# Kernel optimization log

Hardware: AMD Instinct MI355X
Metric: run time of the kernel (lower is better)

The kernel has to match this reference:

```python
import jax, jax.numpy as jnp
import numpy as np

N_RAYS, N_SAMPLES, WIDTH = 4096, 192, 128


def _linear_params(key, fan_in, fan_out):
    # torch nn.Linear default init: U(-1/sqrt(fan_in), 1/sqrt(fan_in))
    kw, kb = jax.random.split(key)
    s = 1.0 / np.sqrt(fan_in)
    w = jax.random.uniform(kw, (fan_in, fan_out), minval=-s, maxval=s, dtype=jnp.float32)
    b = jax.random.uniform(kb, (fan_out,), minval=-s, maxval=s, dtype=jnp.float32)
    return w, b


def setup_inputs() -> dict:
    key = jax.random.key(0)
    ks = jax.random.split(key, 9)
    w0, b0 = _linear_params(ks[0], 3, WIDTH)            # feature layer 0
    w1, b1 = _linear_params(ks[1], WIDTH, WIDTH)        # feature layer 1
    w2, b2 = _linear_params(ks[2], WIDTH + 3, WIDTH)    # feature layer 2 (skip concat)
    w3, b3 = _linear_params(ks[3], WIDTH, WIDTH)        # feature layer 3
    wd, bd = _linear_params(ks[4], WIDTH, 1)            # density head
    wf, bf = _linear_params(ks[5], WIDTH, WIDTH)        # feature head
    wr, br = _linear_params(ks[6], WIDTH + 3, WIDTH // 2)  # rgb layer
    wo, bo = _linear_params(ks[7], WIDTH // 2, 3)       # rgb head
    x = jax.random.normal(ks[8], (N_RAYS, N_SAMPLES, 6), dtype=jnp.float32)
    return dict(x=x, w0=w0, b0=b0, w1=w1, b1=b1, w2=w2, b2=b2, w3=w3, b3=b3,
                wd=wd, bd=bd, wf=wf, bf=bf, wr=wr, br=br, wo=wo, bo=bo)


def reference(x, w0, b0, w1, b1, w2, b2, w3, b3, wd, bd, wf, bf, wr, br, wo, bo):
    relu = jax.nn.relu
    position, view_dir = x[..., :3], x[..., 3:]
    h = relu(position @ w0 + b0)                                   # [R,S,128]
    h = relu(h @ w1 + b1)
    h = relu(jnp.concatenate([h, position], axis=-1) @ w2 + b2)    # skip at i=2
    h = relu(h @ w3 + b3)
    density = relu(h @ wd + bd)                                    # [R,S,1]
    features = relu(h @ wf + bf)                                   # [R,S,128]
    r = relu(jnp.concatenate([features, view_dir], axis=-1) @ wr + br)  # [R,S,64]
    rgb = jax.nn.sigmoid(r @ wo + bo)                              # [R,S,3]
    return (rgb, density)
```

## Files before the change

### kernel.cpp

```cpp
#include <hip/hip_runtime.h>
#include <hip/hip_bf16.h>

#define N_PTS (4096 * 192)
#define NT 4

typedef __bf16 bf16x8 __attribute__((ext_vector_type(8)));
typedef float  f32x4  __attribute__((ext_vector_type(4)));
typedef float  f32x2  __attribute__((ext_vector_type(2)));

#define W1P 0
#define W2P 16384
#define W3P 32768
#define WFP 49152
#define WRP 65536
#define W0E 73728
#define W2E 75776
#define WRE 77824
#define WDE 78848
#define WOE 79104

__device__ __forceinline__ int kinv(int k) {
  int c = k >> 5, q = (k >> 3) & 3, h = (k >> 2) & 1, r = k & 3;
  return (2 * c + h) * 16 + q * 4 + r;
}

__global__ void prep_kernel(const float* __restrict__ w0, const float* __restrict__ w1,
                            const float* __restrict__ w2, const float* __restrict__ w3,
                            const float* __restrict__ wf, const float* __restrict__ wr,
                            const float* __restrict__ wd, const float* __restrict__ wo,
                            __bf16* __restrict__ ws) {
  int i = blockIdx.x * 256 + threadIdx.x;
  if (i < 65536) {
    int t = i >> 14, j = i & 16383, m = j >> 7, col = j & 127;
    int k = (((col >> 3) ^ (m & 15)) << 3) | (col & 7);
    int p = kinv(k);
    const float* w = (t == 0) ? w1 : (t == 1) ? w2 : (t == 2) ? w3 : wf;
    ws[i] = (__bf16)w[p * 128 + m];
  } else if (i < 73728) {
    int j = i - 65536, m = j >> 7, col = j & 127;
    int k = (((col >> 3) ^ (m & 15)) << 3) | (col & 7);
    int p = kinv(k);
    ws[i] = (__bf16)wr[p * 64 + m];
  } else if (i < 75776) {
    int j = i - 73728, f = j >> 4, k = j & 15; float v = 0.f;
    if (k < 3)      v = w0[k * 128 + f];
    else if (k < 6) v = w0[(k - 3) * 128 + f];
    else if (k < 9) { float w = w0[(k - 6) * 128 + f]; v = w - (float)(__bf16)w; }
    ws[i] = (__bf16)v;
  } else if (i < 77824) {
    int j = i - 75776, f = j >> 4, k = j & 15; float v = 0.f;
    if (k < 3)      v = w2[(128 + k) * 128 + f];
    else if (k < 6) v = w2[(128 + k - 3) * 128 + f];
    else if (k < 9) { float w = w2[(128 + k - 6) * 128 + f]; v = w - (float)(__bf16)w; }
    ws[i] = (__bf16)v;
  } else if (i < 78848) {
    int j = i - 77824, n = j >> 4, k = j & 15; float v = 0.f;
    if (k >= 9 && k < 15) v = wr[(128 + ((k - 9) % 3)) * 64 + n];
    ws[i] = (__bf16)v;
  } else if (i < 79104) {
    int j = i - 78848, row = j >> 7, k = j & 127, p = kinv(k);
    float v = wd[p];
    ws[i] = (row == 0) ? (__bf16)v : (__bf16)(v - (float)(__bf16)v);
  } else if (i < 79616) {
    int j = i - 79104, row = j >> 6, k = j & 63, p = kinv(k);
    float v = 0.f;
    if (row < 3)                 v = wo[p * 3 + row];
    else if (row >= 4 && row < 7) { float w = wo[p * 3 + row - 4]; v = w - (float)(__bf16)w; }
    ws[i] = (__bf16)v;
  }
}

__device__ __forceinline__ bf16x8 zero8() {
  bf16x8 z;
#pragma unroll
  for (int i = 0; i < 8; ++i) z[i] = (__bf16)0.f;
  return z;
}

__device__ __forceinline__ bf16x8 pack_relu(f32x4 e, f32x4 o) {
  bf16x8 v;
#pragma unroll
  for (int r = 0; r < 4; ++r) {
    v[r]     = (__bf16)fmaxf(e[r], 0.f);
    v[4 + r] = (__bf16)fmaxf(o[r], 0.f);
  }
  return v;
}

template <int NB>
__device__ __forceinline__ void stage_tile(const __bf16* __restrict__ gsrc,
                                           __bf16* lds, int wv, int lane) {
  const char* g = (const char*)gsrc;
  char* l = (char*)lds;
#pragma unroll
  for (int r = 0; r < NB; r += 4096) {
    const char* src = g + r + wv * 1024 + lane * 16;
    char* dst = l + r + wv * 1024;
    __builtin_amdgcn_global_load_lds(
        (const __attribute__((address_space(1))) void*)src,
        (__attribute__((address_space(3))) void*)dst, 16, 0, 0);
  }
}

template <int NPAIR, bool FIX>
__device__ __forceinline__ void mlayer(const __bf16* __restrict__ wlds,
                                       const float* __restrict__ bias,
                                       const __bf16* __restrict__ wext,
                                       const bf16x8 (&pf)[NT],
                                       const bf16x8 (&hin)[4][NT],
                                       bf16x8 (&hout)[NPAIR][NT],
                                       int l16, int quad) {
#pragma unroll
  for (int pr = 0; pr < NPAIR; ++pr) {
    f32x4 acc0[NT], acc1[NT];
    f32x4 bv0 = *(const f32x4*)(bias + pr * 32 + quad * 4);
    f32x4 bv1 = *(const f32x4*)(bias + pr * 32 + 16 + quad * 4);
#pragma unroll
    for (int nt = 0; nt < NT; ++nt) { acc0[nt] = bv0; acc1[nt] = bv1; }
#pragma unroll
    for (int c = 0; c < 4; ++c) {
      int chunk = ((c * 4 + quad) ^ l16) << 3;
      bf16x8 a0 = *(const bf16x8*)(wlds + (pr * 32 + l16) * 128 + chunk);
      bf16x8 a1 = *(const bf16x8*)(wlds + (pr * 32 + 16 + l16) * 128 + chunk);
#pragma unroll
      for (int nt = 0; nt < NT; ++nt) {
        acc0[nt] = __builtin_amdgcn_mfma_f32_16x16x32_bf16(a0, hin[c][nt], acc0[nt], 0, 0, 0);
        acc1[nt] = __builtin_amdgcn_mfma_f32_16x16x32_bf16(a1, hin[c][nt], acc1[nt], 0, 0, 0);
      }
    }
    if constexpr (FIX) {
      bf16x8 a0 = zero8(), a1 = zero8();
      if (quad < 2) {
        a0 = *(const bf16x8*)(wext + (pr * 32 + l16) * 16 + quad * 8);
        a1 = *(const bf16x8*)(wext + (pr * 32 + 16 + l16) * 16 + quad * 8);
      }
#pragma unroll
      for (int nt = 0; nt < NT; ++nt) {
        acc0[nt] = __builtin_amdgcn_mfma_f32_16x16x32_bf16(a0, pf[nt], acc0[nt], 0, 0, 0);
        acc1[nt] = __builtin_amdgcn_mfma_f32_16x16x32_bf16(a1, pf[nt], acc1[nt], 0, 0, 0);
      }
    }
#pragma unroll
    for (int nt = 0; nt < NT; ++nt) hout[pr][nt] = pack_relu(acc0[nt], acc1[nt]);
  }
}

__global__ __launch_bounds__(256, 2) void nerf_kernel(
    const float* __restrict__ x,
    const float* __restrict__ b0, const float* __restrict__ b1,
    const float* __restrict__ b2, const float* __restrict__ b3,
    const float* __restrict__ bd, const float* __restrict__ bfv,
    const float* __restrict__ br, const float* __restrict__ bo,
    const __bf16* __restrict__ ws,
    float* __restrict__ out) {
  __shared__ __align__(16) __bf16 posb[256 * 16];
  __shared__ __align__(16) __bf16 sA[128 * 128];
  __shared__ __align__(16) __bf16 sB[128 * 128];

  const int tid  = threadIdx.x;
  const int wv   = tid >> 6;
  const int lane = tid & 63;
  const int quad = lane >> 4;
  const int l16  = lane & 15;
  const int p0   = blockIdx.x * 256;
  const int pw   = wv * 64;

  stage_tile<32768>(ws + W1P, sA, wv, lane);
  stage_tile<32768>(ws + W2P, sB, wv, lane);

  {
    const float* xp = x + (size_t)(p0 + tid) * 6;
    f32x2 a = *(const f32x2*)xp;
    f32x2 b = *(const f32x2*)(xp + 2);
    f32x2 c = *(const f32x2*)(xp + 4);
    float px = a[0], py = a[1], pz = b[0], vx = b[1], vy = c[0], vz = c[1];
    __bf16 phx = (__bf16)px, phy = (__bf16)py, phz = (__bf16)pz;
    __bf16 vhx = (__bf16)vx, vhy = (__bf16)vy, vhz = (__bf16)vz;
    __bf16 plx = (__bf16)(px - (float)phx), ply = (__bf16)(py - (float)phy), plz = (__bf16)(pz - (float)phz);
    __bf16 vlx = (__bf16)(vx - (float)vhx), vly = (__bf16)(vy - (float)vhy), vlz = (__bf16)(vz - (float)vhz);
    bf16x8 r0, r1;
    r0[0] = phx; r0[1] = phy; r0[2] = phz; r0[3] = plx; r0[4] = ply; r0[5] = plz; r0[6] = phx; r0[7] = phy;
    r1[0] = phz; r1[1] = vhx; r1[2] = vhy; r1[3] = vhz; r1[4] = vlx; r1[5] = vly; r1[6] = vlz; r1[7] = (__bf16)0.f;
    *(bf16x8*)(posb + tid * 16) = r0;
    *(bf16x8*)(posb + tid * 16 + 8) = r1;
  }

  bf16x8 w0a[4], w0b[4];
#pragma unroll
  for (int pr = 0; pr < 4; ++pr) {
    w0a[pr] = zero8(); w0b[pr] = zero8();
    if (quad < 2) {
      w0a[pr] = *(const bf16x8*)(ws + W0E + (pr * 32 + l16) * 16 + quad * 8);
      w0b[pr] = *(const bf16x8*)(ws + W0E + (pr * 32 + 16 + l16) * 16 + quad * 8);
    }
  }

  bf16x8 pf[NT];
#pragma unroll
  for (int nt = 0; nt < NT; ++nt) {
    pf[nt] = zero8();
    if (quad < 2) pf[nt] = *(const bf16x8*)(posb + (pw + nt * 16 + l16) * 16 + quad * 8);
  }

  bf16x8 hA[4][NT], hB[4][NT];

#pragma unroll
  for (int pr = 0; pr < 4; ++pr) {
    f32x4 acc0[NT], acc1[NT];
    f32x4 bv0 = *(const f32x4*)(b0 + pr * 32 + quad * 4);
    f32x4 bv1 = *(const f32x4*)(b0 + pr * 32 + 16 + quad * 4);
#pragma unroll
    for (int nt = 0; nt < NT; ++nt) { acc0[nt] = bv0; acc1[nt] = bv1; }
#pragma unroll
    for (int nt = 0; nt < NT; ++nt) {
      acc0[nt] = __builtin_amdgcn_mfma_f32_16x16x32_bf16(w0a[pr], pf[nt], acc0[nt], 0, 0, 0);
      acc1[nt] = __builtin_amdgcn_mfma_f32_16x16x32_bf16(w0b[pr], pf[nt], acc1[nt], 0, 0, 0);
    }
#pragma unroll
    for (int nt = 0; nt < NT; ++nt) hA[pr][nt] = pack_relu(acc0[nt], acc1[nt]);
  }
  __syncthreads();

  mlayer<4, false>(sA, b1, nullptr, pf, hA, hB, l16, quad);
  __syncthreads();
  stage_tile<32768>(ws + W3P, sA, wv, lane);

  mlayer<4, true>(sB, b2, ws + W2E, pf, hB, hA, l16, quad);
  __syncthreads();
  stage_tile<32768>(ws + WFP, sB, wv, lane);

  mlayer<4, false>(sA, b3, nullptr, pf, hA, hB, l16, quad);
  __syncthreads();
  stage_tile<16384>(ws + WRP, sA, wv, lane);

  {
    f32x4 accd[NT];
#pragma unroll
    for (int nt = 0; nt < NT; ++nt) accd[nt] = f32x4{0.f, 0.f, 0.f, 0.f};
    int drow = (l16 < 2) ? l16 : 0;
#pragma unroll
    for (int c = 0; c < 4; ++c) {
      bf16x8 ad = *(const bf16x8*)(ws + WDE + drow * 128 + c * 32 + quad * 8);
#pragma unroll
      for (int nt = 0; nt < NT; ++nt)
        accd[nt] = __builtin_amdgcn_mfma_f32_16x16x32_bf16(ad, hB[c][nt], accd[nt], 0, 0, 0);
    }
    float bdv = bd[0];
    if (quad == 0) {
#pragma unroll
      for (int nt = 0; nt < NT; ++nt)
        out[(size_t)3 * N_PTS + p0 + pw + nt * 16 + l16] =
            fmaxf(accd[nt][0] + accd[nt][1] + bdv, 0.f);
    }
  }

  mlayer<4, false>(sB, bfv, nullptr, pf, hB, hA, l16, quad);
  __syncthreads();

  bf16x8 hR[2][NT];
  mlayer<2, true>(sA, br, ws + WRE, pf, hA, hR, l16, quad);

  {
    f32x4 acco[NT];
#pragma unroll
    for (int nt = 0; nt < NT; ++nt) acco[nt] = f32x4{0.f, 0.f, 0.f, 0.f};
    int orow = l16 & 7;
#pragma unroll
    for (int c = 0; c < 2; ++c) {
      bf16x8 ao = *(const bf16x8*)(ws + WOE + orow * 64 + c * 32 + quad * 8);
#pragma unroll
      for (int nt = 0; nt < NT; ++nt)
        acco[nt] = __builtin_amdgcn_mfma_f32_16x16x32_bf16(ao, hR[c][nt], acco[nt], 0, 0, 0);
    }
    float bo0 = bo[0], bo1 = bo[1], bo2 = bo[2];
#pragma unroll
    for (int nt = 0; nt < NT; ++nt) {
      float lo0 = __shfl_xor(acco[nt][0], 16, 64);
      float lo1 = __shfl_xor(acco[nt][1], 16, 64);
      float lo2 = __shfl_xor(acco[nt][2], 16, 64);
      if (quad == 0) {
        size_t o = (size_t)(p0 + pw + nt * 16 + l16) * 3;
        float s0 = acco[nt][0] + lo0 + bo0;
        float s1 = acco[nt][1] + lo1 + bo1;
        float s2 = acco[nt][2] + lo2 + bo2;
        out[o + 0] = 1.f / (1.f + __expf(-s0));
        out[o + 1] = 1.f / (1.f + __expf(-s1));
        out[o + 2] = 1.f / (1.f + __expf(-s2));
      }
    }
  }
}

extern "C" void kernel_launch(void* const* d_in, const int* in_sizes, int n_in,
                              void* d_out, int out_size, void* d_ws, size_t ws_size,
                              hipStream_t stream) {
  const float* x  = (const float*)d_in[0];
  const float* w0 = (const float*)d_in[1];
  const float* b0 = (const float*)d_in[2];
  const float* w1 = (const float*)d_in[3];
  const float* b1 = (const float*)d_in[4];
  const float* w2 = (const float*)d_in[5];
  const float* b2 = (const float*)d_in[6];
  const float* w3 = (const float*)d_in[7];
  const float* b3 = (const float*)d_in[8];
  const float* wd = (const float*)d_in[9];
  const float* bd = (const float*)d_in[10];
  const float* wf = (const float*)d_in[11];
  const float* bfv= (const float*)d_in[12];
  const float* wr = (const float*)d_in[13];
  const float* br = (const float*)d_in[14];
  const float* wo = (const float*)d_in[15];
  const float* bo = (const float*)d_in[16];
  __bf16* ws = (__bf16*)d_ws;
  float* out = (float*)d_out;

  prep_kernel<<<311, 256, 0, stream>>>(w0, w1, w2, w3, wf, wr, wd, wo, ws);
  nerf_kernel<<<N_PTS / 256, 256, 0, stream>>>(x, b0, b1, b2, b3, bd, bfv, br, bo, ws, out);
}
```

Baseline: 202.8 us.

## Switch MLP layers from 16x16x32 to 32x32x16 bf16 MFMA tiles

Replaces the 16x16x32 MFMA tiling with 32x32x16 bf16 MFMA, so each wave computes 32-row by 32-point tiles. The weight-permutation helper, LDS reads, activation register layout and head reductions are all remapped to fit the new operand layout. The aim is fewer MFMA issues and fewer LDS weight fetches per FLOP, and the K=3/6 skip inputs no longer need padding to K=32. The cost is larger accumulators (16 floats each), which may raise register pressure at 2 blocks per CU.

```diff
diff --git a/kernel.cpp b/kernel.cpp
--- a/kernel.cpp
+++ b/kernel.cpp
@@ -2,9 +2,9 @@
 #include <hip/hip_bf16.h>
 
 #define N_PTS (4096 * 192)
-#define NT 4
 
 typedef __bf16 bf16x8 __attribute__((ext_vector_type(8)));
+typedef float  f32x16 __attribute__((ext_vector_type(16)));
 typedef float  f32x4  __attribute__((ext_vector_type(4)));
 typedef float  f32x2  __attribute__((ext_vector_type(2)));
 
@@ -20,8 +20,9 @@
 #define WOE 79104
 
 __device__ __forceinline__ int kinv(int k) {
-  int c = k >> 5, q = (k >> 3) & 3, h = (k >> 2) & 1, r = k & 3;
-  return (2 * c + h) * 16 + q * 4 + r;
+  int c = k >> 4, h = (k >> 3) & 1, e = k & 7;
+  int mt = c >> 1, q = (c & 1) * 2 + (e >> 2), r = e & 3;
+  return mt * 32 + q * 8 + h * 4 + r;
 }
 
 __global__ void prep_kernel(const float* __restrict__ w0, const float* __restrict__ w1,
@@ -70,20 +71,11 @@
   }
 }
 
-__device__ __forceinline__ bf16x8 zero8() {
-  bf16x8 z;
-#pragma unroll
-  for (int i = 0; i < 8; ++i) z[i] = (__bf16)0.f;
-  return z;
-}
-
-__device__ __forceinline__ bf16x8 pack_relu(f32x4 e, f32x4 o) {
+template <int BASE>
+__device__ __forceinline__ bf16x8 pack_relu(const f32x16& a) {
   bf16x8 v;
 #pragma unroll
-  for (int r = 0; r < 4; ++r) {
-    v[r]     = (__bf16)fmaxf(e[r], 0.f);
-    v[4 + r] = (__bf16)fmaxf(o[r], 0.f);
-  }
+  for (int r = 0; r < 8; ++r) v[r] = (__bf16)fmaxf(a[BASE + r], 0.f);
   return v;
 }
 
@@ -102,46 +94,39 @@
   }
 }
 
-template <int NPAIR, bool FIX>
+template <int NM, bool FIX>
 __device__ __forceinline__ void mlayer(const __bf16* __restrict__ wlds,
                                        const float* __restrict__ bias,
                                        const __bf16* __restrict__ wext,
-                                       const bf16x8 (&pf)[NT],
-                                       const bf16x8 (&hin)[4][NT],
-                                       bf16x8 (&hout)[NPAIR][NT],
-                                       int l16, int quad) {
-#pragma unroll
-  for (int pr = 0; pr < NPAIR; ++pr) {
-    f32x4 acc0[NT], acc1[NT];
-    f32x4 bv0 = *(const f32x4*)(bias + pr * 32 + quad * 4);
-    f32x4 bv1 = *(const f32x4*)(bias + pr * 32 + 16 + quad * 4);
-#pragma unroll
-    for (int nt = 0; nt < NT; ++nt) { acc0[nt] = bv0; acc1[nt] = bv1; }
-#pragma unroll
-    for (int c = 0; c < 4; ++c) {
-      int chunk = ((c * 4 + quad) ^ l16) << 3;
-      bf16x8 a0 = *(const bf16x8*)(wlds + (pr * 32 + l16) * 128 + chunk);
-      bf16x8 a1 = *(const bf16x8*)(wlds + (pr * 32 + 16 + l16) * 128 + chunk);
-#pragma unroll
-      for (int nt = 0; nt < NT; ++nt) {
-        acc0[nt] = __builtin_amdgcn_mfma_f32_16x16x32_bf16(a0, hin[c][nt], acc0[nt], 0, 0, 0);
-        acc1[nt] = __builtin_amdgcn_mfma_f32_16x16x32_bf16(a1, hin[c][nt], acc1[nt], 0, 0, 0);
-      }
+                                       const bf16x8 (&pf)[2],
+                                       const bf16x8 (&hin)[8][2],
+                                       bf16x8 (&hout)[2 * NM][2],
+                                       int row, int h) {
+#pragma unroll
+  for (int mt = 0; mt < NM; ++mt) {
+    f32x16 a0, a1;
+#pragma unroll
+    for (int q = 0; q < 4; ++q) {
+      f32x4 bv = *(const f32x4*)(bias + mt * 32 + q * 8 + h * 4);
+#pragma unroll
+      for (int r = 0; r < 4; ++r) { a0[q * 4 + r] = bv[r]; a1[q * 4 + r] = bv[r]; }
+    }
+#pragma unroll
+    for (int c = 0; c < 8; ++c) {
+      bf16x8 w = *(const bf16x8*)(wlds + (mt * 32 + row) * 128 +
+                                  (((c * 2 + h) ^ (row & 15)) << 3));
+      a0 = __builtin_amdgcn_mfma_f32_32x32x16_bf16(w, hin[c][0], a0, 0, 0, 0);
+      a1 = __builtin_amdgcn_mfma_f32_32x32x16_bf16(w, hin[c][1], a1, 0, 0, 0);
     }
     if constexpr (FIX) {
-      bf16x8 a0 = zero8(), a1 = zero8();
-      if (quad < 2) {
-        a0 = *(const bf16x8*)(wext + (pr * 32 + l16) * 16 + quad * 8);
-        a1 = *(const bf16x8*)(wext + (pr * 32 + 16 + l16) * 16 + quad * 8);
-      }
-#pragma unroll
-      for (int nt = 0; nt < NT; ++nt) {
-        acc0[nt] = __builtin_amdgcn_mfma_f32_16x16x32_bf16(a0, pf[nt], acc0[nt], 0, 0, 0);
-        acc1[nt] = __builtin_amdgcn_mfma_f32_16x16x32_bf16(a1, pf[nt], acc1[nt], 0, 0, 0);
-      }
-    }
-#pragma unroll
-    for (int nt = 0; nt < NT; ++nt) hout[pr][nt] = pack_relu(acc0[nt], acc1[nt]);
+      bf16x8 w = *(const bf16x8*)(wext + (mt * 32 + row) * 16 + h * 8);
+      a0 = __builtin_amdgcn_mfma_f32_32x32x16_bf16(w, pf[0], a0, 0, 0, 0);
+      a1 = __builtin_amdgcn_mfma_f32_32x32x16_bf16(w, pf[1], a1, 0, 0, 0);
+    }
+    hout[2 * mt][0]     = pack_relu<0>(a0);
+    hout[2 * mt + 1][0] = pack_relu<8>(a0);
+    hout[2 * mt][1]     = pack_relu<0>(a1);
+    hout[2 * mt + 1][1] = pack_relu<8>(a1);
   }
 }
 
@@ -160,8 +145,8 @@
   const int tid  = threadIdx.x;
   const int wv   = tid >> 6;
   const int lane = tid & 63;
-  const int quad = lane >> 4;
-  const int l16  = lane & 15;
+  const int row  = lane & 31;
+  const int h    = lane >> 5;
   const int p0   = blockIdx.x * 256;
   const int pw   = wv * 64;
 
@@ -185,108 +170,99 @@
     *(bf16x8*)(posb + tid * 16 + 8) = r1;
   }
 
-  bf16x8 w0a[4], w0b[4];
-#pragma unroll
-  for (int pr = 0; pr < 4; ++pr) {
-    w0a[pr] = zero8(); w0b[pr] = zero8();
-    if (quad < 2) {
-      w0a[pr] = *(const bf16x8*)(ws + W0E + (pr * 32 + l16) * 16 + quad * 8);
-      w0b[pr] = *(const bf16x8*)(ws + W0E + (pr * 32 + 16 + l16) * 16 + quad * 8);
-    }
-  }
-
-  bf16x8 pf[NT];
-#pragma unroll
-  for (int nt = 0; nt < NT; ++nt) {
-    pf[nt] = zero8();
-    if (quad < 2) pf[nt] = *(const bf16x8*)(posb + (pw + nt * 16 + l16) * 16 + quad * 8);
-  }
-
-  bf16x8 hA[4][NT], hB[4][NT];
-
-#pragma unroll
-  for (int pr = 0; pr < 4; ++pr) {
-    f32x4 acc0[NT], acc1[NT];
-    f32x4 bv0 = *(const f32x4*)(b0 + pr * 32 + quad * 4);
-    f32x4 bv1 = *(const f32x4*)(b0 + pr * 32 + 16 + quad * 4);
-#pragma unroll
-    for (int nt = 0; nt < NT; ++nt) { acc0[nt] = bv0; acc1[nt] = bv1; }
-#pragma unroll
-    for (int nt = 0; nt < NT; ++nt) {
-      acc0[nt] = __builtin_amdgcn_mfma_f32_16x16x32_bf16(w0a[pr], pf[nt], acc0[nt], 0, 0, 0);
-      acc1[nt] = __builtin_amdgcn_mfma_f32_16x16x32_bf16(w0b[pr], pf[nt], acc1[nt], 0, 0, 0);
-    }
-#pragma unroll
-    for (int nt = 0; nt < NT; ++nt) hA[pr][nt] = pack_relu(acc0[nt], acc1[nt]);
-  }
-  __syncthreads();
-
-  mlayer<4, false>(sA, b1, nullptr, pf, hA, hB, l16, quad);
+  bf16x8 w0f[4];
+#pragma unroll
+  for (int mt = 0; mt < 4; ++mt)
+    w0f[mt] = *(const bf16x8*)(ws + W0E + (mt * 32 + row) * 16 + h * 8);
+
+  bf16x8 pf[2];
+#pragma unroll
+  for (int nt = 0; nt < 2; ++nt)
+    pf[nt] = *(const bf16x8*)(posb + (pw + nt * 32 + row) * 16 + h * 8);
+
+  bf16x8 hA[8][2], hB[8][2];
+
+#pragma unroll
+  for (int mt = 0; mt < 4; ++mt) {
+    f32x16 a0, a1;
+#pragma unroll
+    for (int q = 0; q < 4; ++q) {
+      f32x4 bv = *(const f32x4*)(b0 + mt * 32 + q * 8 + h * 4);
+#pragma unroll
+      for (int r = 0; r < 4; ++r) { a0[q * 4 + r] = bv[r]; a1[q * 4 + r] = bv[r]; }
+    }
+    a0 = __builtin_amdgcn_mfma_f32_32x32x16_bf16(w0f[mt], pf[0], a0, 0, 0, 0);
+    a1 = __builtin_amdgcn_mfma_f32_32x32x16_bf16(w0f[mt], pf[1], a1, 0, 0, 0);
+    hA[2 * mt][0]     = pack_relu<0>(a0);
+    hA[2 * mt + 1][0] = pack_relu<8>(a0);
+    hA[2 * mt][1]     = pack_relu<0>(a1);
+    hA[2 * mt + 1][1] = pack_relu<8>(a1);
+  }
+  __syncthreads();
+
+  mlayer<4, false>(sA, b1, nullptr, pf, hA, hB, row, h);
   __syncthreads();
   stage_tile<32768>(ws + W3P, sA, wv, lane);
 
-  mlayer<4, true>(sB, b2, ws + W2E, pf, hB, hA, l16, quad);
+  mlayer<4, true>(sB, b2, ws + W2E, pf, hB, hA, row, h);
   __syncthreads();
   stage_tile<32768>(ws + WFP, sB, wv, lane);
 
-  mlayer<4, false>(sA, b3, nullptr, pf, hA, hB, l16, quad);
+  mlayer<4, false>(sA, b3, nullptr, pf, hA, hB, row, h);
   __syncthreads();
   stage_tile<16384>(ws + WRP, sA, wv, lane);
 
   {
-    f32x4 accd[NT];
-#pragma unroll
-    for (int nt = 0; nt < NT; ++nt) accd[nt] = f32x4{0.f, 0.f, 0.f, 0.f};
-    int drow = (l16 < 2) ? l16 : 0;
+    f32x16 a0, a1;
+#pragma unroll
+    for (int r = 0; r < 16; ++r) { a0[r] = 0.f; a1[r] = 0.f; }
+    int dr = (row == 1) ? 128 : 0;
+#pragma unroll
+    for (int c = 0; c < 8; ++c) {
+      bf16x8 ad = *(const bf16x8*)(ws + WDE + dr + c * 16 + h * 8);
+      a0 = __builtin_amdgcn_mfma_f32_32x32x16_bf16(ad, hB[c][0], a0, 0, 0, 0);
+      a1 = __builtin_amdgcn_mfma_f32_32x32x16_bf16(ad, hB[c][1], a1, 0, 0, 0);
+    }
+    if (h == 0) {
+      float bdv = bd[0];
+      out[(size_t)3 * N_PTS + p0 + pw + row]      = fmaxf(a0[0] + a0[1] + bdv, 0.f);
+      out[(size_t)3 * N_PTS + p0 + pw + 32 + row] = fmaxf(a1[0] + a1[1] + bdv, 0.f);
+    }
+  }
+
+  mlayer<4, false>(sB, bfv, nullptr, pf, hB, hA, row, h);
+  __syncthreads();
+
+  bf16x8 hR[4][2];
+  mlayer<2, true>(sA, br, ws + WRE, pf, hA, hR, row, h);
+
+  {
+    f32x16 a0, a1;
+#pragma unroll
+    for (int r = 0; r < 16; ++r) { a0[r] = 0.f; a1[r] = 0.f; }
+    int orow = (row & 7) * 64;
 #pragma unroll
     for (int c = 0; c < 4; ++c) {
-      bf16x8 ad = *(const bf16x8*)(ws + WDE + drow * 128 + c * 32 + quad * 8);
-#pragma unroll
-      for (int nt = 0; nt < NT; ++nt)
-        accd[nt] = __builtin_amdgcn_mfma_f32_16x16x32_bf16(ad, hB[c][nt], accd[nt], 0, 0, 0);
-    }
-    float bdv = bd[0];
-    if (quad == 0) {
-#pragma unroll
-      for (int nt = 0; nt < NT; ++nt)
-        out[(size_t)3 * N_PTS + p0 + pw + nt * 16 + l16] =
-            fmaxf(accd[nt][0] + accd[nt][1] + bdv, 0.f);
-    }
-  }
-
-  mlayer<4, false>(sB, bfv, nullptr, pf, hB, hA, l16, quad);
-  __syncthreads();
-
-  bf16x8 hR[2][NT];
-  mlayer<2, true>(sA, br, ws + WRE, pf, hA, hR, l16, quad);
-
-  {
-    f32x4 acco[NT];
-#pragma unroll
-    for (int nt = 0; nt < NT; ++nt) acco[nt] = f32x4{0.f, 0.f, 0.f, 0.f};
-    int orow = l16 & 7;
-#pragma unroll
-    for (int c = 0; c < 2; ++c) {
-      bf16x8 ao = *(const bf16x8*)(ws + WOE + orow * 64 + c * 32 + quad * 8);
-#pragma unroll
-      for (int nt = 0; nt < NT; ++nt)
-        acco[nt] = __builtin_amdgcn_mfma_f32_16x16x32_bf16(ao, hR[c][nt], acco[nt], 0, 0, 0);
-    }
-    float bo0 = bo[0], bo1 = bo[1], bo2 = bo[2];
-#pragma unroll
-    for (int nt = 0; nt < NT; ++nt) {
-      float lo0 = __shfl_xor(acco[nt][0], 16, 64);
-      float lo1 = __shfl_xor(acco[nt][1], 16, 64);
-      float lo2 = __shfl_xor(acco[nt][2], 16, 64);
-      if (quad == 0) {
-        size_t o = (size_t)(p0 + pw + nt * 16 + l16) * 3;
-        float s0 = acco[nt][0] + lo0 + bo0;
-        float s1 = acco[nt][1] + lo1 + bo1;
-        float s2 = acco[nt][2] + lo2 + bo2;
-        out[o + 0] = 1.f / (1.f + __expf(-s0));
-        out[o + 1] = 1.f / (1.f + __expf(-s1));
-        out[o + 2] = 1.f / (1.f + __expf(-s2));
-      }
+      bf16x8 ao = *(const bf16x8*)(ws + WOE + orow + c * 16 + h * 8);
+      a0 = __builtin_amdgcn_mfma_f32_32x32x16_bf16(ao, hR[c][0], a0, 0, 0, 0);
+      a1 = __builtin_amdgcn_mfma_f32_32x32x16_bf16(ao, hR[c][1], a1, 0, 0, 0);
+    }
+    float s00 = a0[0] + __shfl_xor(a0[0], 32, 64);
+    float s01 = a0[1] + __shfl_xor(a0[1], 32, 64);
+    float s02 = a0[2] + __shfl_xor(a0[2], 32, 64);
+    float s10 = a1[0] + __shfl_xor(a1[0], 32, 64);
+    float s11 = a1[1] + __shfl_xor(a1[1], 32, 64);
+    float s12 = a1[2] + __shfl_xor(a1[2], 32, 64);
+    if (h == 0) {
+      float bo0 = bo[0], bo1 = bo[1], bo2 = bo[2];
+      size_t o0 = (size_t)(p0 + pw + row) * 3;
+      out[o0 + 0] = 1.f / (1.f + __expf(-(s00 + bo0)));
+      out[o0 + 1] = 1.f / (1.f + __expf(-(s01 + bo1)));
+      out[o0 + 2] = 1.f / (1.f + __expf(-(s02 + bo2)));
+      size_t o1 = (size_t)(p0 + pw + 32 + row) * 3;
+      out[o1 + 0] = 1.f / (1.f + __expf(-(s10 + bo0)));
+      out[o1 + 1] = 1.f / (1.f + __expf(-(s11 + bo1)));
+      out[o1 + 2] = 1.f / (1.f + __expf(-(s12 + bo2)));
     }
   }
 }
```

New measurement: 216.3 us. 1.07x slower.
